# Optimization experiments

Measured on AMD Instinct MI355X. Metric: run time of the kernel, lower is better.

Reference implementation:

```python
import jax, jax.numpy as jnp
import numpy as np

DIM = 4096
N_HEADS = 32
N_KV_HEADS = 8
HEAD_DIM = DIM // N_HEADS  # 128
N_REP = N_HEADS // N_KV_HEADS  # 4
THETA = 10000.0
B, S = 4, 1024


def setup_inputs() -> dict:
    key = jax.random.key(0)
    ks = jax.random.split(key, 5)
    sc = 1.0 / np.sqrt(DIM).astype(np.float32)
    x = jax.random.normal(ks[0], (B, S, DIM), jnp.float32)
    wq = jax.random.normal(ks[1], (DIM, N_HEADS * HEAD_DIM), jnp.float32) * sc
    wk = jax.random.normal(ks[2], (DIM, N_KV_HEADS * HEAD_DIM), jnp.float32) * sc
    wv = jax.random.normal(ks[3], (DIM, N_KV_HEADS * HEAD_DIM), jnp.float32) * sc
    wo = jax.random.normal(ks[4], (N_HEADS * HEAD_DIM, DIM), jnp.float32) * sc
    return {"x": x, "wq": wq, "wk": wk, "wv": wv, "wo": wo}


def _rope_cos_sin(seq_len):
    # matches precompute_freqs_cis: freqs over even indices, angles = t * freqs
    freqs = 1.0 / (THETA ** (jnp.arange(0, HEAD_DIM, 2, dtype=jnp.float32) / HEAD_DIM))
    t = jnp.arange(seq_len, dtype=jnp.float32)
    ang = jnp.outer(t, freqs)  # [S, HEAD_DIM//2]
    return jnp.cos(ang), jnp.sin(ang)


def _apply_rope(x, cos, sin):
    # x: [B, S, H, D]; consecutive pairs form complex numbers (view_as_complex)
    xr = x[..., 0::2]
    xi = x[..., 1::2]
    c = cos[None, :, None, :]
    s = sin[None, :, None, :]
    out_r = xr * c - xi * s
    out_i = xr * s + xi * c
    return jnp.stack([out_r, out_i], axis=-1).reshape(x.shape)


def reference(x, wq, wk, wv, wo):
    bsz, seq_len, _ = x.shape
    q = (x @ wq).reshape(bsz, seq_len, N_HEADS, HEAD_DIM)
    k = (x @ wk).reshape(bsz, seq_len, N_KV_HEADS, HEAD_DIM)
    v = (x @ wv).reshape(bsz, seq_len, N_KV_HEADS, HEAD_DIM)
    cos, sin = _rope_cos_sin(seq_len)
    q = _apply_rope(q, cos, sin)
    k = _apply_rope(k, cos, sin)
    # repeat_kv: expand each kv head N_REP times contiguously
    k = jnp.repeat(k, N_REP, axis=2)
    v = jnp.repeat(v, N_REP, axis=2)
    scores = jnp.einsum('bqhd,bkhd->bhqk', q, k) / np.float32(np.sqrt(HEAD_DIM))
    mask = jnp.triu(jnp.full((seq_len, seq_len), -jnp.inf, dtype=scores.dtype), k=1)
    scores = scores + mask
    attn = jax.nn.softmax(scores.astype(jnp.float32), axis=-1).astype(q.dtype)
    out = jnp.einsum('bhqk,bkhd->bqhd', attn, v).reshape(bsz, seq_len, N_HEADS * HEAD_DIM)
    return out @ wo
```

## Files before the change

kernel.cpp:

```cpp
#include <hip/hip_runtime.h>

typedef unsigned short u16;
typedef unsigned int u32;
typedef __attribute__((ext_vector_type(8))) short short8_t;
typedef __attribute__((ext_vector_type(4))) float f32x4;

static constexpr int Bc = 4, Sc = 1024, Hc = 32, HKVc = 8, Dc = 128;
static constexpr int BS = Bc * Sc;
static constexpr int DIMc = 4096;

__device__ __forceinline__ u16 f2bf(float f) {
  u32 u = __float_as_uint(f);
  u32 r = (u + 0x7fffu + ((u >> 16) & 1u)) >> 16;
  return (u16)r;
}
__device__ __forceinline__ float bf2f(u16 u) {
  return __uint_as_float(((u32)u) << 16);
}
__device__ __forceinline__ void gload_lds16(const void* g, void* l) {
  __builtin_amdgcn_global_load_lds((const __attribute__((address_space(1))) void*)g,
                                   (__attribute__((address_space(3))) void*)l, 16, 0, 0);
}

#define SBAR __builtin_amdgcn_sched_barrier(0)
#define PBARRIER do { SBAR; __builtin_amdgcn_s_barrier(); SBAR; } while (0)
#define WAITVM(N) asm volatile("s_waitcnt vmcnt(" #N ")" ::: "memory")

__global__ void rope_table_k(float* __restrict__ tbl) {
  int i = blockIdx.x * 256 + threadIdx.x;
  int s = i >> 6, fi = i & 63;
  float freq = powf(10000.f, -(float)fi / 64.f);
  float ang = (float)s * freq;
  float sv, cv;
  sincosf(ang, &sv, &cv);
  tbl[2 * i] = cv;
  tbl[2 * i + 1] = sv;
}

__global__ void f32_to_bf16_k(const float* __restrict__ in, u16* __restrict__ out, int n4) {
  int i = blockIdx.x * 256 + threadIdx.x;
  if (i >= n4) return;
  float4 v = *(const float4*)(in + (size_t)i * 4);
  uint2 pk;
  pk.x = (u32)f2bf(v.x) | ((u32)f2bf(v.y) << 16);
  pk.y = (u32)f2bf(v.z) | ((u32)f2bf(v.w) << 16);
  *(uint2*)(out + (size_t)i * 4) = pk;
}

__global__ __launch_bounds__(256) void transpose_w_k(const float* __restrict__ W, u16* __restrict__ WT,
                                                     int Kdim, int Ndim) {
  __shared__ float tile[64 * 65];
  const int t = threadIdx.x;
  const int n0 = blockIdx.x * 64, k0 = blockIdx.y * 64;
  #pragma unroll
  for (int p = 0; p < 4; ++p) {
    int idx = p * 256 + t;
    int r = idx >> 4, c = (idx & 15) * 4;
    float4 v = *(const float4*)(W + (size_t)(k0 + r) * Ndim + n0 + c);
    tile[r * 65 + c + 0] = v.x;
    tile[r * 65 + c + 1] = v.y;
    tile[r * 65 + c + 2] = v.z;
    tile[r * 65 + c + 3] = v.w;
  }
  __syncthreads();
  #pragma unroll
  for (int p = 0; p < 2; ++p) {
    int idx = p * 256 + t;
    int n = idx >> 3, c = (idx & 7) * 8;
    alignas(16) u16 o[8];
    #pragma unroll
    for (int i = 0; i < 8; ++i) o[i] = f2bf(tile[(c + i) * 65 + n]);
    *(uint4*)(WT + (size_t)(n0 + n) * Kdim + k0 + c) = *(const uint4*)o;
  }
}

#define MFMAQ(QI, AF, BF)                                                                \
  do {                                                                                   \
    __builtin_amdgcn_s_setprio(1);                                                       \
    _Pragma("unroll") for (int mf = 0; mf < 4; ++mf)                                     \
      _Pragma("unroll") for (int nf = 0; nf < 2; ++nf)                                   \
        _Pragma("unroll") for (int kk = 0; kk < 2; ++kk)                                 \
          acc[QI][mf][nf] = __builtin_amdgcn_mfma_f32_16x16x32_bf16(                     \
              AF[mf][kk], BF[nf][kk], acc[QI][mf][nf], 0, 0, 0);                         \
    __builtin_amdgcn_s_setprio(0);                                                       \
  } while (0)

template <int MODE>
__global__ __launch_bounds__(512, 2) void gemm256(const u16* __restrict__ A, const u16* __restrict__ BT,
                                                  void* __restrict__ Cv, const float* __restrict__ tbl,
                                                  int M, int N, int K) {
  extern __shared__ char smem[];
  const int t = threadIdx.x, l = t & 63, w = t >> 6;
  const int ln15 = l & 15, lh = l >> 4;
  const int NT = K >> 6;

  int id = blockIdx.x;
  int nwg = gridDim.x;
  int swz = ((nwg & 7) == 0) ? ((id & 7) * (nwg >> 3) + (id >> 3)) : id;
  const int nbn = N >> 8;
  const int bm = swz / nbn, bn = swz % nbn;

  const u16* Ag = A + (size_t)bm * 256 * K;
  const u16* Bg = BT + (size_t)bn * 256 * K;

  f32x4 acc[4][4][2];
  #pragma unroll
  for (int q = 0; q < 4; ++q)
    #pragma unroll
    for (int mf = 0; mf < 4; ++mf)
      #pragma unroll
      for (int nf = 0; nf < 2; ++nf) acc[q][mf][nf] = f32x4{0.f, 0.f, 0.f, 0.f};
  short8_t af[4][2], af2[4][2], bfB0[2][2], bfB1[2][2];

  const int srow = (l >> 3);
  const int sck  = (l & 7) ^ srow;
  auto stageA = [&](char* bufbase, int h, int tt) {
    char* lb = bufbase + h * 16384 + w * 1024;
    const u16* g = Ag + (size_t)(h * 128 + w * 8 + srow) * K + tt * 64 + (sck << 3);
    gload_lds16(g, lb);
    gload_lds16(g + (size_t)64 * K, lb + 8192);
  };
  auto stageB = [&](char* bufbase, int h, int tt) {
    char* lb = bufbase + 32768 + h * 16384 + w * 1024;
    const u16* g = Bg + (size_t)(h * 128 + w * 8 + srow) * K + tt * 64 + (sck << 3);
    gload_lds16(g, lb);
    gload_lds16(g + (size_t)64 * K, lb + 8192);
  };
  const int arow = (w >> 2) * 64 + ln15;
  const int brow = (w & 3) * 32 + ln15;
  const int rsw = ln15 & 7;
  auto LDA = [&](const char* cb, int qm, short8_t (&dst)[4][2]) {
    #pragma unroll
    for (int mf = 0; mf < 4; ++mf)
      #pragma unroll
      for (int kk = 0; kk < 2; ++kk)
        dst[mf][kk] = *(const short8_t*)(cb + qm * 16384 + (arow + mf * 16) * 128 +
                                         (((kk * 4 + lh) ^ rsw) << 4));
  };
  auto LDB = [&](const char* cb, int qn, short8_t (&dst)[2][2]) {
    #pragma unroll
    for (int nf = 0; nf < 2; ++nf)
      #pragma unroll
      for (int kk = 0; kk < 2; ++kk)
        dst[nf][kk] = *(const short8_t*)(cb + 32768 + qn * 16384 + (brow + nf * 16) * 128 +
                                         (((kk * 4 + lh) ^ rsw) << 4));
  };

  stageA(smem, 0, 0);
  stageB(smem, 0, 0);
  stageB(smem, 1, 0);
  stageA(smem, 1, 0);
  WAITVM(2);
  PBARRIER;

  for (int T = 0; T < NT; ++T) {
    char* cb = smem + (T & 1) * 65536;
    char* nb = smem + ((T & 1) ^ 1) * 65536;
    const bool s1 = (T + 1 < NT);
    LDB(cb, 0, bfB0);
    LDB(cb, 1, bfB1);
    if (s1) {
      stageA(nb, 0, T + 1);
      stageB(nb, 0, T + 1);
      stageB(nb, 1, T + 1);
      stageA(nb, 1, T + 1);
    }
    LDA(cb, 0, af);
    MFMAQ(0, af, bfB0);
    MFMAQ(3, af, bfB1);
    if (s1) { WAITVM(8); } else { WAITVM(0); }
    LDA(cb, 1, af2);
    MFMAQ(1, af2, bfB0);
    MFMAQ(2, af2, bfB1);
    if (s1) { WAITVM(2); }
    PBARRIER;
  }

  const int rw = (w >> 2) * 64, cw = (w & 3) * 32;
  #pragma unroll
  for (int qi = 0; qi < 4; ++qi) {
    const int qm = (qi == 1 || qi == 2) ? 1 : 0;
    const int qn = (qi >= 2) ? 1 : 0;
    #pragma unroll
    for (int mf = 0; mf < 4; ++mf)
      #pragma unroll
      for (int nf = 0; nf < 2; ++nf)
        #pragma unroll
        for (int e = 0; e < 4; ++e) {
          int row = bm * 256 + qm * 128 + rw + mf * 16 + lh * 4 + e;
          int col = bn * 256 + qn * 128 + cw + nf * 16 + ln15;
          float v = acc[qi][mf][nf][e];
          if (MODE == 2) {
            float pv = __shfl_xor(v, 1);
            int d = col & 127, hh = col >> 7;
            int s = row & (Sc - 1), bb = row >> 10;
            float2 cs = *(const float2*)(tbl + (size_t)(s * 64 + (d >> 1)) * 2);
            float o = (d & 1) ? (v * cs.x + pv * cs.y) : (v * cs.x - pv * cs.y);
            o *= 0.08838834764831845f;
            ((u16*)Cv)[(((size_t)(bb * Hc + hh) * Sc + s) << 7) + d] = f2bf(o);
          } else {
            size_t idx = (size_t)row * N + col;
            ((float*)Cv)[idx] = v;
          }
        }
  }
}

#define MFMAKV(QM, AF)                                                                   \
  do {                                                                                   \
    __builtin_amdgcn_s_setprio(1);                                                       \
    _Pragma("unroll") for (int mf = 0; mf < 4; ++mf)                                     \
      _Pragma("unroll") for (int nf = 0; nf < 2; ++nf)                                   \
        _Pragma("unroll") for (int kk = 0; kk < 2; ++kk)                                 \
          acc[QM][mf][nf] = __builtin_amdgcn_mfma_f32_16x16x32_bf16(                     \
              AF[mf][kk], bf[nf][kk], acc[QM][mf][nf], 0, 0, 0);                         \
    __builtin_amdgcn_s_setprio(0);                                                       \
  } while (0)

__global__ __launch_bounds__(512, 1) void gemm_kv(const u16* __restrict__ A, const u16* __restrict__ BT,
                                                  u16* __restrict__ Krp, u16* __restrict__ Vtp,
                                                  const float* __restrict__ tbl) {
  extern __shared__ char smem[];
  const int t = threadIdx.x, l = t & 63, w = t >> 6;
  const int ln15 = l & 15, lh = l >> 4;
  const int K = 4096, NT = 64;

  int id = blockIdx.x;
  int swz = (id & 7) * 32 + (id >> 3);
  const int bm = swz >> 4, bn = swz & 15;

  const u16* Ag = A + (size_t)bm * 256 * K;
  const u16* Bg = BT + (size_t)bn * 128 * K;

  f32x4 acc[2][4][2];
  #pragma unroll
  for (int q = 0; q < 2; ++q)
    #pragma unroll
    for (int mf = 0; mf < 4; ++mf)
      #pragma unroll
      for (int nf = 0; nf < 2; ++nf) acc[q][mf][nf] = f32x4{0.f, 0.f, 0.f, 0.f};
  short8_t af[4][2], af2[4][2], bf[2][2];

  const int srow = (l >> 3);
  const int sck  = (l & 7) ^ srow;
  auto stageA = [&](int buf, int h, int tt) {
    char* lb = smem + buf * 32768 + h * 16384 + w * 2048;
    const u16* g = Ag + (size_t)(h * 128 + w * 16 + srow) * K + tt * 64 + (sck << 3);
    gload_lds16(g, lb);
    gload_lds16(g + (size_t)8 * K, lb + 1024);
  };
  auto stageB = [&](int buf, int tt) {
    char* lb = smem + 65536 + buf * 16384 + w * 2048;
    const u16* g = Bg + (size_t)(w * 16 + srow) * K + tt * 64 + (sck << 3);
    gload_lds16(g, lb);
    gload_lds16(g + (size_t)8 * K, lb + 1024);
  };
  const int arow = (w >> 2) * 64 + ln15;
  const int brow = (w & 3) * 32 + ln15;
  const int rsw = ln15 & 7;
  auto LDA = [&](int buf, int qm, short8_t (&dst)[4][2]) {
    #pragma unroll
    for (int mf = 0; mf < 4; ++mf)
      #pragma unroll
      for (int kk = 0; kk < 2; ++kk)
        dst[mf][kk] = *(const short8_t*)(smem + buf * 32768 + qm * 16384 + (arow + mf * 16) * 128 +
                                         (((kk * 4 + lh) ^ rsw) << 4));
  };
  auto LDB = [&](int buf) {
    #pragma unroll
    for (int nf = 0; nf < 2; ++nf)
      #pragma unroll
      for (int kk = 0; kk < 2; ++kk)
        bf[nf][kk] = *(const short8_t*)(smem + 65536 + buf * 16384 + (brow + nf * 16) * 128 +
                                        (((kk * 4 + lh) ^ rsw) << 4));
  };

  stageA(0, 0, 0);
  stageB(0, 0);
  stageA(0, 1, 0);
  WAITVM(2);
  PBARRIER;

  for (int T = 0; T < NT; ++T) {
    const int cb = T & 1, nb = cb ^ 1;
    const bool st = (T + 1 < NT);
    LDB(cb);
    if (st) { stageA(nb, 0, T + 1); stageB(nb, T + 1); stageA(nb, 1, T + 1); }
    LDA(cb, 0, af);
    MFMAKV(0, af);
    if (st) { WAITVM(6); } else { WAITVM(0); }
    LDA(cb, 1, af2);
    MFMAKV(1, af2);
    if (st) { WAITVM(2); }
    PBARRIER;
  }

  #pragma unroll
  for (int qm = 0; qm < 2; ++qm)
    #pragma unroll
    for (int mf = 0; mf < 4; ++mf)
      #pragma unroll
      for (int nf = 0; nf < 2; ++nf)
        #pragma unroll
        for (int e = 0; e < 4; ++e) {
          int row = bm * 256 + qm * 128 + (w >> 2) * 64 + mf * 16 + lh * 4 + e;
          int col = bn * 128 + (w & 3) * 32 + nf * 16 + ln15;
          float v = acc[qm][mf][nf][e];
          float pv = __shfl_xor(v, 1);
          int s = row & (Sc - 1), bb = row >> 10;
          if (col < 1024) {
            int hkv = col >> 7, d = col & 127;
            float2 cs = *(const float2*)(tbl + (size_t)(s * 64 + (d >> 1)) * 2);
            float o = (d & 1) ? (v * cs.x + pv * cs.y) : (v * cs.x - pv * cs.y);
            Krp[(((size_t)(bb * HKVc + hkv) * Sc + s) << 7) + d] = f2bf(o);
          } else {
            int vc = col - 1024;
            int hkv = vc >> 7, d = vc & 127;
            int sl = s & 63;
            int sg = (sl & 32) | (((sl >> 2) & 3) << 3) | (((sl >> 4) & 1) << 2) | (sl & 3);
            Vtp[((size_t)(bb * HKVc + hkv) * Dc + d) * Sc + (s & ~63) + sg] = f2bf(v);
          }
        }
}

__global__ __launch_bounds__(512, 4) void attn_k(const u16* __restrict__ Q, const u16* __restrict__ Kr,
                                                 const u16* __restrict__ Vt, u16* __restrict__ AO) {
  extern __shared__ char smem[];
  const int t = threadIdx.x, l = t & 63, w = t >> 6;
  const int qb = (int)gridDim.x - 1 - (int)blockIdx.x;
  const int h = blockIdx.y, b = blockIdx.z;
  const int hkv = h >> 2;
  const int ln15 = l & 15, lh = l >> 4;
  const int NT = 2 * qb + 2;

  const u16* Kg0 = Kr + (size_t)(b * HKVc + hkv) * Sc * Dc;
  const u16* Vg0 = Vt + (size_t)(b * HKVc + hkv) * Dc * Sc;

  auto stageK = [&](int buf, int tt) {
    char* base = smem + buf * 16384 + w * 2048;
    #pragma unroll
    for (int i = 0; i < 2; ++i) {
      int row = w * 8 + i * 4 + (l >> 4);
      int c = l & 15;
      gload_lds16(Kg0 + (size_t)(tt * 64 + row) * Dc + ((c ^ (row & 7)) << 3), base + i * 1024);
    }
  };
  auto stageV = [&](int buf, int tt) {
    char* base = smem + 32768 + buf * 16384 + w * 2048;
    #pragma unroll
    for (int i = 0; i < 2; ++i) {
      int d = w * 16 + i * 8 + (l >> 3);
      int c = l & 7;
      gload_lds16(Vg0 + (size_t)d * Sc + tt * 64 + ((c ^ (d & 7)) << 3), base + i * 1024);
    }
  };

  short8_t qf[4];
  {
    int q = qb * 128 + w * 16 + ln15;
    const u16* qp = Q + ((size_t)(b * Hc + h) * Sc + q) * Dc + lh * 8;
    #pragma unroll
    for (int ks = 0; ks < 4; ++ks) qf[ks] = *(const short8_t*)(qp + ks * 32);
  }
  SBAR;

  f32x4 oacc[8];
  #pragma unroll
  for (int i = 0; i < 8; ++i) oacc[i] = f32x4{0.f, 0.f, 0.f, 0.f};
  float mrun = -1e30f, lrun = 0.f;

  stageK(0, 0); stageV(0, 0);
  stageK(1, 1); stageV(1, 1);

  const int qmaxw = qb * 128 + w * 16 + 15;
  const int qlane = qb * 128 + w * 16 + ln15;

  for (int T = 0; T < NT; ++T) {
    if (T < NT - 1) { WAITVM(4); } else { WAITVM(0); }
    PBARRIER;
    const char* Kb = smem + (T & 1) * 16384;
    const char* Vb = smem + 32768 + (T & 1) * 16384;

    if (T * 64 <= qmaxw) {
      f32x4 sf[4];
      #pragma unroll
      for (int fc = 0; fc < 4; ++fc) {
        sf[fc] = f32x4{0.f, 0.f, 0.f, 0.f};
        int kvr = fc * 16 + ln15;
        #pragma unroll
        for (int ks = 0; ks < 4; ++ks) {
          int chunk = ks * 4 + lh;
          short8_t kf = *(const short8_t*)(Kb + kvr * 256 + ((chunk ^ (kvr & 7)) << 4));
          sf[fc] = __builtin_amdgcn_mfma_f32_16x16x32_bf16(kf, qf[ks], sf[fc], 0, 0, 0);
        }
      }
      if (T * 64 + 63 > qb * 128 + w * 16) {
        #pragma unroll
        for (int fc = 0; fc < 4; ++fc)
          #pragma unroll
          for (int j = 0; j < 4; ++j) {
            int kvg = T * 64 + fc * 16 + lh * 4 + j;
            if (kvg > qlane) sf[fc][j] = -1e30f;
          }
      }
      float mx = sf[0][0];
      #pragma unroll
      for (int fc = 0; fc < 4; ++fc)
        #pragma unroll
        for (int j = 0; j < 4; ++j) mx = fmaxf(mx, sf[fc][j]);
      mx = fmaxf(mx, __shfl_xor(mx, 16));
      mx = fmaxf(mx, __shfl_xor(mx, 32));
      float mnew = fmaxf(mrun, mx);
      float alpha = __expf(mrun - mnew);
      mrun = mnew;
      float rs = 0.f;
      #pragma unroll
      for (int fc = 0; fc < 4; ++fc)
        #pragma unroll
        for (int j = 0; j < 4; ++j) {
          float p = __expf(sf[fc][j] - mnew);
          sf[fc][j] = p;
          rs += p;
        }
      rs += __shfl_xor(rs, 16);
      rs += __shfl_xor(rs, 32);
      lrun = lrun * alpha + rs;
      float arow[4];
      #pragma unroll
      for (int j = 0; j < 4; ++j) arow[j] = __shfl(alpha, (l & 48) | (lh * 4 + j));
      #pragma unroll
      for (int fd = 0; fd < 8; ++fd)
        #pragma unroll
        for (int j = 0; j < 4; ++j) oacc[fd][j] *= arow[j];
      short8_t pa[2];
      #pragma unroll
      for (int ks = 0; ks < 2; ++ks)
        #pragma unroll
        for (int b2 = 0; b2 < 2; ++b2)
          #pragma unroll
          for (int j = 0; j < 4; ++j) pa[ks][b2 * 4 + j] = (short)f2bf(sf[ks * 2 + b2][j]);
      #pragma unroll
      for (int fd = 0; fd < 8; ++fd) {
        int dcol = fd * 16 + ln15;
        #pragma unroll
        for (int ks = 0; ks < 2; ++ks) {
          int chunk = ks * 4 + lh;
          short8_t vf = *(const short8_t*)(Vb + dcol * 128 + ((chunk ^ (dcol & 7)) << 4));
          oacc[fd] = __builtin_amdgcn_mfma_f32_16x16x32_bf16(pa[ks], vf, oacc[fd], 0, 0, 0);
        }
      }
    }
    PBARRIER;
    if (T + 2 < NT) { stageK(T & 1, T + 2); stageV(T & 1, T + 2); }
  }

  float linv[4];
  #pragma unroll
  for (int j = 0; j < 4; ++j) linv[j] = 1.f / __shfl(lrun, (l & 48) | (lh * 4 + j));
  #pragma unroll
  for (int j = 0; j < 4; ++j) {
    int q = qb * 128 + w * 16 + lh * 4 + j;
    u16* op = AO + (size_t)(b * Sc + q) * DIMc + h * Dc + ln15;
    #pragma unroll
    for (int fd = 0; fd < 8; ++fd) op[fd * 16] = f2bf(oacc[fd][j] * linv[j]);
  }
}

extern "C" void kernel_launch(void* const* d_in, const int* in_sizes, int n_in,
                              void* d_out, int out_size, void* d_ws, size_t ws_size,
                              hipStream_t stream) {
  const float* x  = (const float*)d_in[0];
  const float* wq = (const float*)d_in[1];
  const float* wk = (const float*)d_in[2];
  const float* wv = (const float*)d_in[3];
  const float* wo = (const float*)d_in[4];
  float* out = (float*)d_out;

  char* ws = (char*)d_ws;
  size_t off = 0;
  auto alloc = [&](size_t bytes) -> char* {
    char* p = ws + off;
    off += (bytes + 255) & ~(size_t)255;
    return p;
  };
  float* tbl  = (float*)alloc((size_t)Sc * 64 * 2 * 4);
  u16* xb    = (u16*)alloc((size_t)BS * DIMc * 2);
  u16* wqT   = (u16*)alloc((size_t)4096 * 4096 * 2);
  u16* wkvT  = (u16*)alloc((size_t)2048 * 4096 * 2);
  u16* Qb    = (u16*)alloc((size_t)BS * 4096 * 2);
  u16* Krp   = (u16*)alloc((size_t)BS * 1024 * 2);
  u16* Vtp   = (u16*)alloc((size_t)BS * 1024 * 2);
  u16* AO = xb;
  u16* woT = wqT;

  rope_table_k<<<(Sc * 64) / 256, 256, 0, stream>>>(tbl);
  f32_to_bf16_k<<<(BS * DIMc / 4) / 256, 256, 0, stream>>>(x, xb, BS * DIMc / 4);

  transpose_w_k<<<dim3(64, 64), 256, 0, stream>>>(wq, wqT, 4096, 4096);
  gemm256<2><<<256, 512, 131072, stream>>>(xb, wqT, Qb, tbl, 4096, 4096, 4096);

  transpose_w_k<<<dim3(16, 64), 256, 0, stream>>>(wk, wkvT, 4096, 1024);
  transpose_w_k<<<dim3(16, 64), 256, 0, stream>>>(wv, wkvT + (size_t)1024 * 4096, 4096, 1024);
  gemm_kv<<<256, 512, 98304, stream>>>(xb, wkvT, Krp, Vtp, tbl);

  attn_k<<<dim3(8, Hc, Bc), 512, 65536, stream>>>(Qb, Krp, Vtp, AO);

  transpose_w_k<<<dim3(64, 64), 256, 0, stream>>>(wo, woT, 4096, 4096);
  gemm256<1><<<256, 512, 131072, stream>>>(AO, woT, out, tbl, 4096, 4096, 4096);
}
```

Before: 473.2 us.

## Restructure GEMM main loop into 8-phase ping-pong with two-tile-ahead prefetch

Prefetches two K-tiles ahead into the double buffer. Each quarter of the current buffer is refilled for tile T+2 as soon as its fragments have been read into registers. The loop is split into barrier-separated phases that interleave LDS reads, global-to-LDS staging and MFMA quadrants. The aim is to hide more global-load latency and keep the loads and matrix math overlapping, at the cost of more workgroup barriers per iteration. It also depends on careful vmcnt accounting for correctness.

```diff
diff --git a/kernel.cpp b/kernel.cpp
--- a/kernel.cpp
+++ b/kernel.cpp
@@ -146,33 +146,37 @@
                                          (((kk * 4 + lh) ^ rsw) << 4));
   };
 
-  stageA(smem, 0, 0);
-  stageB(smem, 0, 0);
-  stageB(smem, 1, 0);
-  stageA(smem, 1, 0);
-  WAITVM(2);
+  {
+    char* b0 = smem;
+    char* b1 = smem + 65536;
+    stageA(b0, 0, 0); stageB(b0, 0, 0); stageA(b0, 1, 0); stageB(b0, 1, 0);
+    stageA(b1, 0, 1); stageB(b1, 0, 1); stageA(b1, 1, 1); stageB(b1, 1, 1);
+  }
+  WAITVM(8);
   PBARRIER;
 
   for (int T = 0; T < NT; ++T) {
     char* cb = smem + (T & 1) * 65536;
-    char* nb = smem + ((T & 1) ^ 1) * 65536;
-    const bool s1 = (T + 1 < NT);
-    LDB(cb, 0, bfB0);
+    const bool s2 = (T + 2 < NT);
+    LDA(cb, 0, af); LDB(cb, 0, bfB0);
+    PBARRIER;
+    MFMAQ(0, af, bfB0);
+    PBARRIER;
+    LDA(cb, 1, af2);
+    if (s2) { stageA(cb, 0, T + 2); stageB(cb, 0, T + 2); }
+    PBARRIER;
+    MFMAQ(1, af2, bfB0);
+    PBARRIER;
     LDB(cb, 1, bfB1);
-    if (s1) {
-      stageA(nb, 0, T + 1);
-      stageB(nb, 0, T + 1);
-      stageB(nb, 1, T + 1);
-      stageA(nb, 1, T + 1);
-    }
-    LDA(cb, 0, af);
-    MFMAQ(0, af, bfB0);
+    if (s2) stageA(cb, 1, T + 2);
+    PBARRIER;
+    MFMAQ(2, af2, bfB1);
+    PBARRIER;
+    if (s2) stageB(cb, 1, T + 2);
+    if (s2)               { WAITVM(8); }
+    else if (T + 1 < NT)  { WAITVM(0); }
+    PBARRIER;
     MFMAQ(3, af, bfB1);
-    if (s1) { WAITVM(8); } else { WAITVM(0); }
-    LDA(cb, 1, af2);
-    MFMAQ(1, af2, bfB0);
-    MFMAQ(2, af2, bfB1);
-    if (s1) { WAITVM(2); }
     PBARRIER;
   }
 
```

After: 480.7 us. Within noise of the previous version (+1.6%).
